# Kernel tuning notes

Hardware: AMD Instinct MI355X
Metric: run time of the kernel (lower is better)

## Reference

```python
import jax, jax.numpy as jnp
import numpy as np
import math

BT, N, D, H = 16, 1024, 128, 8
HD = D // H


def setup_inputs() -> dict:
    key = jax.random.key(0)
    ks = jax.random.split(key, 12)
    s = 1.0 / math.sqrt(D)
    return {
        "x": jax.random.normal(ks[0], (BT, N, D), dtype=jnp.float32),
        "adj": jax.random.uniform(ks[1], (BT, N, N), dtype=jnp.float32),
        "Wq": jax.random.normal(ks[2], (D, D), dtype=jnp.float32) * s,
        "bq": jax.random.normal(ks[3], (D,), dtype=jnp.float32) * 0.01,
        "Wk": jax.random.normal(ks[4], (D, D), dtype=jnp.float32) * s,
        "bk": jax.random.normal(ks[5], (D,), dtype=jnp.float32) * 0.01,
        "Wv": jax.random.normal(ks[6], (D, D), dtype=jnp.float32) * s,
        "bv": jax.random.normal(ks[7], (D,), dtype=jnp.float32) * 0.01,
        "Wo": jax.random.normal(ks[8], (D, D), dtype=jnp.float32) * s,
        "bo": jax.random.normal(ks[9], (D,), dtype=jnp.float32) * 0.01,
    }


def reference(x, adj, Wq, bq, Wk, bk, Wv, bv, Wo, bo):
    bt, n, d = x.shape
    # projections (torch Linear: x @ W.T + b), split into heads -> (BT,H,N,HD)
    q = (x @ Wq.T + bq).reshape(bt, n, H, HD).transpose(0, 2, 1, 3)
    k = (x @ Wk.T + bk).reshape(bt, n, H, HD).transpose(0, 2, 1, 3)
    v = (x @ Wv.T + bv).reshape(bt, n, H, HD).transpose(0, 2, 1, 3)
    scores = jnp.einsum('bhnd,bhmd->bhnm', q, k) / math.sqrt(HD)  # (BT,H,N,N)
    mask = (adj == 0)[:, None, :, :]  # (BT,1,N,N)
    scores = jnp.where(mask, -jnp.inf, scores)
    attn = jax.nn.softmax(scores, axis=-1)
    attn = attn * adj[:, None, :, :]  # reweight by continuous causal strength
    attn = attn / (attn.sum(axis=-1, keepdims=True) + 1e-8)  # renormalize
    ctx = jnp.einsum('bhnm,bhmd->bhnd', attn, v)  # (BT,H,N,HD)
    ctx = ctx.transpose(0, 2, 1, 3).reshape(bt, n, d)
    return ctx @ Wo.T + bo
```

## Files before the change

### kernel.cpp

```cpp
#include <hip/hip_runtime.h>
#include <hip/hip_bf16.h>

#define BTC 16
#define NC 1024
#define DC 128
#define HC 8
#define HDC 16

typedef __attribute__((ext_vector_type(8))) short bf16x8;
typedef __attribute__((ext_vector_type(4))) float f32x4;
typedef __attribute__((ext_vector_type(16))) float f32x16;
typedef __attribute__((ext_vector_type(4))) short short4v;

#if __has_builtin(__builtin_amdgcn_exp2f)
#define EXP2F(x) __builtin_amdgcn_exp2f(x)
#else
#define EXP2F(x) exp2f(x)
#endif

#define QSCALE 0.36067376022224085f

union PK2 { short4v s4; __hip_bfloat162 h2[2]; };
union PK8 { bf16x8 v; short s[8]; __hip_bfloat162 h2[4]; };

static __device__ inline short f2bf(float f) {
    unsigned u = __builtin_bit_cast(unsigned, f);
    u += 0x7fffu + ((u >> 16) & 1u);
    return (short)(u >> 16);
}

#define LDS_BARRIER()                                              \
    do {                                                           \
        asm volatile("s_waitcnt lgkmcnt(0)" ::: "memory");         \
        __builtin_amdgcn_s_barrier();                              \
        asm volatile("" ::: "memory");                             \
    } while (0)

__global__ __launch_bounds__(256)
void prep_kernel(const float* __restrict__ x,
                 const float* __restrict__ Wq, const float* __restrict__ Wk,
                 const float* __restrict__ Wv, const float* __restrict__ Wo,
                 short* __restrict__ xbf, short* __restrict__ Wbf)
{
    int gid  = blockIdx.x * 256 + threadIdx.x;
    int base = gid * 4;
    const float* src;
    short* dst;
    if (base < 2097152) {
        src = x + base; dst = xbf + base;
    } else {
        int idx = base - 2097152;
        int w   = idx >> 14;
        int off = idx & 16383;
        src = ((w == 0) ? Wq : (w == 1) ? Wk : (w == 2) ? Wv : Wo) + off;
        dst = Wbf + w * 16384 + off;
    }
    float4 v = *(const float4*)src;
    PK2 pk;
    pk.h2[0] = __float22bfloat162_rn(make_float2(v.x, v.y));
    pk.h2[1] = __float22bfloat162_rn(make_float2(v.z, v.w));
    *(short4v*)dst = pk.s4;
}

__global__ __launch_bounds__(256)
void proj_qkv(const short* __restrict__ xbf, const short* __restrict__ Wbf,
              const float* __restrict__ bq, const float* __restrict__ bk,
              const float* __restrict__ bv,
              short* __restrict__ qo, short* __restrict__ ko, short* __restrict__ vto)
{
    __shared__ short T[128 * 72];

    const int y = blockIdx.y;
    const short* W = Wbf + y * 16384;
    const float* bias = (y == 0) ? bq : (y == 1) ? bk : bv;
    const float scale = (y == 0) ? QSCALE : 1.0f;

    const int tid  = threadIdx.x;
    const int wave = tid >> 6;
    const int lane = tid & 63;
    const int l15  = lane & 15;
    const int quad = lane >> 4;
    const int rowA = blockIdx.x * 64 + wave * 16;

    f32x4 acc[8];
#pragma unroll
    for (int t = 0; t < 8; ++t) acc[t] = (f32x4){0.f, 0.f, 0.f, 0.f};

#pragma unroll
    for (int kk = 0; kk < DC; kk += 32) {
        bf16x8 Af = *(const bf16x8*)&xbf[(size_t)(rowA + l15) * DC + kk + quad * 8];
#pragma unroll
        for (int t = 0; t < 8; ++t) {
            bf16x8 Bf = *(const bf16x8*)&W[(t * 16 + l15) * DC + kk + quad * 8];
            acc[t] = __builtin_amdgcn_mfma_f32_16x16x32_bf16(Af, Bf, acc[t], 0, 0, 0);
        }
    }

    if (y == 2) {
#pragma unroll
        for (int t = 0; t < 8; ++t) {
            int c = t * 16 + l15;
            float b = bias[c];
            PK2 pk;
            pk.h2[0] = __float22bfloat162_rn(make_float2(acc[t][0] + b, acc[t][1] + b));
            pk.h2[1] = __float22bfloat162_rn(make_float2(acc[t][2] + b, acc[t][3] + b));
            *(short4v*)&T[c * 72 + wave * 16 + quad * 4] = pk.s4;
        }
        __syncthreads();
        const int bt = blockIdx.x >> 4;
        const int n0 = (blockIdx.x * 64) & 1023;
        const int chunk = tid & 7;
        const int dr    = tid >> 3;
#pragma unroll
        for (int rep = 0; rep < 4; ++rep) {
            int d = rep * 32 + dr;
            bf16x8 u = *(const bf16x8*)&T[d * 72 + chunk * 8];
            *(bf16x8*)&vto[((size_t)bt * DC + d) * NC + n0 + chunk * 8] = u;
        }
    } else {
        short* dst = (y == 0) ? qo : ko;
#pragma unroll
        for (int t = 0; t < 8; ++t) {
            int c  = t * 16 + l15;
            int hh = c >> 4, dd = c & 15;
            float b = bias[c];
#pragma unroll
            for (int r = 0; r < 4; ++r) {
                int row = rowA + quad * 4 + r;
                int btq = row >> 10, n = row & 1023;
                float val = (acc[t][r] + b) * scale;
                dst[(((size_t)btq * HC + hh) * NC + n) * HDC + dd] = f2bf(val);
            }
        }
    }
}

__global__ __launch_bounds__(256)
void proj_out(const short* __restrict__ cbf, const short* __restrict__ Wobf,
              const float* __restrict__ bo, float* __restrict__ out)
{
    const int tid  = threadIdx.x;
    const int wave = tid >> 6;
    const int lane = tid & 63;
    const int l15  = lane & 15;
    const int quad = lane >> 4;
    const int rowA = blockIdx.x * 64 + wave * 16;

    f32x4 acc[8];
#pragma unroll
    for (int t = 0; t < 8; ++t) acc[t] = (f32x4){0.f, 0.f, 0.f, 0.f};

#pragma unroll
    for (int kk = 0; kk < DC; kk += 32) {
        bf16x8 Af = *(const bf16x8*)&cbf[(size_t)(rowA + l15) * DC + kk + quad * 8];
#pragma unroll
        for (int t = 0; t < 8; ++t) {
            bf16x8 Bf = *(const bf16x8*)&Wobf[(t * 16 + l15) * DC + kk + quad * 8];
            acc[t] = __builtin_amdgcn_mfma_f32_16x16x32_bf16(Af, Bf, acc[t], 0, 0, 0);
        }
    }

#pragma unroll
    for (int t = 0; t < 8; ++t) {
        int c = t * 16 + l15;
        float b = bo[c];
#pragma unroll
        for (int r = 0; r < 4; ++r) {
            int row = rowA + quad * 4 + r;
            out[(size_t)row * DC + c] = acc[t][r] + b;
        }
    }
}

__global__ __launch_bounds__(256, 4)
void attn_kernel(const short* __restrict__ qh, const short* __restrict__ kh,
                 const short* __restrict__ vt, const float* __restrict__ adj,
                 short* __restrict__ cb)
{
    __shared__ float As[2][32 * 36];
    __shared__ short Ps[4][2][32 * 40];

    const int tid  = threadIdx.x;
    const int wave = tid >> 6;
    const int lane = tid & 63;
    const int l31  = lane & 31;
    const int hi   = lane >> 5;
    const int l15  = lane & 15;
    const int quad = lane >> 4;
    const int bt   = blockIdx.y;
    const int qt0  = blockIdx.x * 32;
    const int h    = blockIdx.z * 4 + wave;

    const size_t xb = (size_t)bt * NC * DC;
    const size_t hb = ((size_t)bt * HC + h) * NC;

    const short* kp = kh + (hb + l31) * HDC + hi * 8;
    const short* vp = vt + ((size_t)bt * DC + h * HDC + l15) * NC;
    const bf16x8 Bq = *(const bf16x8*)&qh[(hb + qt0 + l31) * HDC + hi * 8];

    const int arow = tid >> 3;
    const int acol = (tid & 7) * 4;
    const float* aptr = adj + (size_t)bt * NC * NC + (size_t)(qt0 + arow) * NC + acol;
    const int awoff = arow * 36 + acol;

    PK8 ones;
#pragma unroll
    for (int j = 0; j < 8; ++j) ones.s[j] = (short)0x3F80;

    f32x16 Z16;
#pragma unroll
    for (int i = 0; i < 16; ++i) Z16[i] = 0.f;

    f32x4 Cc[2], Cw[2];
#pragma unroll
    for (int s = 0; s < 2; ++s) {
        Cc[s] = (f32x4){0.f, 0.f, 0.f, 0.f};
        Cw[s] = (f32x4){0.f, 0.f, 0.f, 0.f};
    }

    short* Pa = &Ps[wave][0][0];
    short* Pb = &Ps[wave][1][0];

    float4 ar = *(const float4*)aptr;
    bf16x8 Ak = *(const bf16x8*)&kp[0];
    bf16x8 Bv = *(const bf16x8*)&vp[quad * 8];
    bf16x8 Bvp;

#define EXPTILE(ASB, PDST)                                                    \
    do {                                                                      \
        const float* asb = (ASB) + l31 * 36 + hi * 4;                         \
        float4 a0 = *(const float4*)&asb[0];                                  \
        float4 a1 = *(const float4*)&asb[8];                                  \
        float4 a2 = *(const float4*)&asb[16];                                 \
        float4 a3 = *(const float4*)&asb[24];                                 \
        short* pd = (PDST) + l31 * 40 + hi * 4;                               \
        PK2 pk;                                                               \
        pk.h2[0] = __float22bfloat162_rn(                                     \
            make_float2(EXP2F(S[0]) * a0.x, EXP2F(S[1]) * a0.y));             \
        pk.h2[1] = __float22bfloat162_rn(                                     \
            make_float2(EXP2F(S[2]) * a0.z, EXP2F(S[3]) * a0.w));             \
        *(short4v*)&pd[0] = pk.s4;                                            \
        pk.h2[0] = __float22bfloat162_rn(                                     \
            make_float2(EXP2F(S[4]) * a1.x, EXP2F(S[5]) * a1.y));             \
        pk.h2[1] = __float22bfloat162_rn(                                     \
            make_float2(EXP2F(S[6]) * a1.z, EXP2F(S[7]) * a1.w));             \
        *(short4v*)&pd[8] = pk.s4;                                            \
        pk.h2[0] = __float22bfloat162_rn(                                     \
            make_float2(EXP2F(S[8]) * a2.x, EXP2F(S[9]) * a2.y));             \
        pk.h2[1] = __float22bfloat162_rn(                                     \
            make_float2(EXP2F(S[10]) * a2.z, EXP2F(S[11]) * a2.w));           \
        *(short4v*)&pd[16] = pk.s4;                                           \
        pk.h2[0] = __float22bfloat162_rn(                                     \
            make_float2(EXP2F(S[12]) * a3.x, EXP2F(S[13]) * a3.y));           \
        pk.h2[1] = __float22bfloat162_rn(                                     \
            make_float2(EXP2F(S[14]) * a3.z, EXP2F(S[15]) * a3.w));           \
        *(short4v*)&pd[24] = pk.s4;                                           \
    } while (0)

    *(float4*)((char*)&As[0][0] + 0 + awoff * 4) = ar;
    ar = *(const float4*)(aptr + 32);
    LDS_BARRIER();

    {
        *(float4*)&As[1][awoff] = ar;
        ar = *(const float4*)(aptr + 64);
        bf16x8 Akn = *(const bf16x8*)&kp[32 * HDC];
        bf16x8 Bvn = *(const bf16x8*)&vp[32 + quad * 8];
        f32x16 S = __builtin_amdgcn_mfma_f32_32x32x16_bf16(Ak, Bq, Z16, 0, 0, 0);
        EXPTILE(&As[0][0], Pa);
        LDS_BARRIER();
        { short* t = Pa; Pa = Pb; Pb = t; }
        Ak = Akn; Bvp = Bv; Bv = Bvn;
    }

#pragma unroll 2
    for (int it = 1; it < 32; ++it) {
        const int jt  = it * 32;
        const int cur = it & 1;

        *(float4*)&As[cur ^ 1][awoff] = ar;
        ar = *(const float4*)(aptr + ((jt + 64) & (NC - 1)));

        bf16x8 Akn = *(const bf16x8*)&kp[((jt + 32) & (NC - 1)) * HDC];
        bf16x8 Bvn = *(const bf16x8*)&vp[((jt + 32) & (NC - 1)) + quad * 8];

        bf16x8 Ap0 = *(const bf16x8*)&Pb[l15 * 40 + quad * 8];
        bf16x8 Ap1 = *(const bf16x8*)&Pb[(16 + l15) * 40 + quad * 8];

        f32x16 S = __builtin_amdgcn_mfma_f32_32x32x16_bf16(Ak, Bq, Z16, 0, 0, 0);

        __builtin_amdgcn_s_setprio(1);
        Cc[0] = __builtin_amdgcn_mfma_f32_16x16x32_bf16(Ap0, Bvp, Cc[0], 0, 0, 0);
        Cw[0] = __builtin_amdgcn_mfma_f32_16x16x32_bf16(Ap0, ones.v, Cw[0], 0, 0, 0);
        Cc[1] = __builtin_amdgcn_mfma_f32_16x16x32_bf16(Ap1, Bvp, Cc[1], 0, 0, 0);
        Cw[1] = __builtin_amdgcn_mfma_f32_16x16x32_bf16(Ap1, ones.v, Cw[1], 0, 0, 0);
        __builtin_amdgcn_s_setprio(0);

        EXPTILE(&As[cur][0], Pa);
        LDS_BARRIER();

        { short* t = Pa; Pa = Pb; Pb = t; }
        Ak = Akn; Bvp = Bv; Bv = Bvn;
    }

    {
        bf16x8 Ap0 = *(const bf16x8*)&Pb[l15 * 40 + quad * 8];
        bf16x8 Ap1 = *(const bf16x8*)&Pb[(16 + l15) * 40 + quad * 8];
        Cc[0] = __builtin_amdgcn_mfma_f32_16x16x32_bf16(Ap0, Bvp, Cc[0], 0, 0, 0);
        Cw[0] = __builtin_amdgcn_mfma_f32_16x16x32_bf16(Ap0, ones.v, Cw[0], 0, 0, 0);
        Cc[1] = __builtin_amdgcn_mfma_f32_16x16x32_bf16(Ap1, Bvp, Cc[1], 0, 0, 0);
        Cw[1] = __builtin_amdgcn_mfma_f32_16x16x32_bf16(Ap1, ones.v, Cw[1], 0, 0, 0);
    }

#pragma unroll
    for (int s = 0; s < 2; ++s)
#pragma unroll
        for (int r = 0; r < 4; ++r) {
            float den = Cw[s][r];
            float rcp = den > 0.f ? 1.f / den : 0.f;
            int row = qt0 + s * 16 + quad * 4 + r;
            cb[xb + (size_t)row * DC + h * HDC + l15] = f2bf(Cc[s][r] * rcp);
        }
#undef EXPTILE
}

extern "C" void kernel_launch(void* const* d_in, const int* in_sizes, int n_in,
                              void* d_out, int out_size, void* d_ws, size_t ws_size,
                              hipStream_t stream)
{
    const float* x   = (const float*)d_in[0];
    const float* adj = (const float*)d_in[1];
    const float* Wq  = (const float*)d_in[2];
    const float* bq  = (const float*)d_in[3];
    const float* Wk  = (const float*)d_in[4];
    const float* bk  = (const float*)d_in[5];
    const float* Wv  = (const float*)d_in[6];
    const float* bv  = (const float*)d_in[7];
    const float* Wo  = (const float*)d_in[8];
    const float* bo  = (const float*)d_in[9];
    float* out = (float*)d_out;

    const size_t tok = (size_t)BTC * NC * DC;
    short* xbf  = (short*)d_ws;
    short* Wbf  = xbf  + tok;
    short* qbuf = Wbf  + 65536;
    short* kbuf = qbuf + tok;
    short* vt   = kbuf + tok;
    short* cbuf = vt   + tok;

    prep_kernel<<<2112, 256, 0, stream>>>(x, Wq, Wk, Wv, Wo, xbf, Wbf);

    dim3 pgrid(256, 3);
    proj_qkv<<<pgrid, 256, 0, stream>>>(xbf, Wbf, bq, bk, bv, qbuf, kbuf, vt);

    dim3 agrid(32, 16, 2);
    attn_kernel<<<agrid, 256, 0, stream>>>(qbuf, kbuf, vt, adj, cbuf);

    proj_out<<<256, 256, 0, stream>>>(cbuf, Wbf + 3 * 16384, bo, out);
}
```

Before: 174.6 us.

## Process 64-key tiles per iteration with single P buffer and fewer barriers

Widens the attention inner loop from 32 to 64 keys per iteration. It computes two score MFMAs and two exp tiles per step and halves the iteration count, and with it the number of LDS barriers. The double-buffered P tile becomes a single wider per-wave buffer. V fragments are now loaded within the same iteration instead of being prefetched one step ahead, and the adj prefetch distance changes. This raises register and LDS use per block, which may reduce occupancy or expose V load latency.

```diff
diff --git a/kernel.cpp b/kernel.cpp
--- a/kernel.cpp
+++ b/kernel.cpp
@@ -177,8 +177,8 @@
                  const short* __restrict__ vt, const float* __restrict__ adj,
                  short* __restrict__ cb)
 {
-    __shared__ float As[2][32 * 36];
-    __shared__ short Ps[4][2][32 * 40];
+    __shared__ float As[2][32 * 68];
+    __shared__ short Ps[4][32 * 72];
 
     const int tid  = threadIdx.x;
     const int wave = tid >> 6;
@@ -199,9 +199,9 @@
     const bf16x8 Bq = *(const bf16x8*)&qh[(hb + qt0 + l31) * HDC + hi * 8];
 
     const int arow = tid >> 3;
-    const int acol = (tid & 7) * 4;
-    const float* aptr = adj + (size_t)bt * NC * NC + (size_t)(qt0 + arow) * NC + acol;
-    const int awoff = arow * 36 + acol;
+    const int acolf = (tid & 7) * 8;
+    const float* aptr = adj + (size_t)bt * NC * NC + (size_t)(qt0 + arow) * NC + acolf;
+    const int awoff = arow * 68 + acolf;
 
     PK8 ones;
 #pragma unroll
@@ -218,22 +218,16 @@
         Cw[s] = (f32x4){0.f, 0.f, 0.f, 0.f};
     }
 
-    short* Pa = &Ps[wave][0][0];
-    short* Pb = &Ps[wave][1][0];
-
-    float4 ar = *(const float4*)aptr;
-    bf16x8 Ak = *(const bf16x8*)&kp[0];
-    bf16x8 Bv = *(const bf16x8*)&vp[quad * 8];
-    bf16x8 Bvp;
-
-#define EXPTILE(ASB, PDST)                                                    \
+    short* Pw = &Ps[wave][0];
+
+#define EXPTILE(S, ASB, H2)                                                   \
     do {                                                                      \
-        const float* asb = (ASB) + l31 * 36 + hi * 4;                         \
+        const float* asb = (ASB) + l31 * 68 + (H2) + hi * 4;                  \
         float4 a0 = *(const float4*)&asb[0];                                  \
         float4 a1 = *(const float4*)&asb[8];                                  \
         float4 a2 = *(const float4*)&asb[16];                                 \
         float4 a3 = *(const float4*)&asb[24];                                 \
-        short* pd = (PDST) + l31 * 40 + hi * 4;                               \
+        short* pd = Pw + l31 * 72 + (H2) + hi * 4;                            \
         PK2 pk;                                                               \
         pk.h2[0] = __float22bfloat162_rn(                                     \
             make_float2(EXP2F(S[0]) * a0.x, EXP2F(S[1]) * a0.y));             \
@@ -257,59 +251,90 @@
         *(short4v*)&pd[24] = pk.s4;                                           \
     } while (0)
 
-    *(float4*)((char*)&As[0][0] + 0 + awoff * 4) = ar;
-    ar = *(const float4*)(aptr + 32);
+    float4 p0a = *(const float4*)&aptr[0];
+    float4 p0b = *(const float4*)&aptr[4];
+    float4 ara = *(const float4*)&aptr[64];
+    float4 arb = *(const float4*)&aptr[68];
+    bf16x8 AkA = *(const bf16x8*)&kp[0];
+    bf16x8 AkB = *(const bf16x8*)&kp[32 * HDC];
+
+    *(float4*)((char*)&As[0][0] + awoff * 4)      = p0a;
+    *(float4*)((char*)&As[0][0] + awoff * 4 + 16) = p0b;
     LDS_BARRIER();
 
     {
-        *(float4*)&As[1][awoff] = ar;
-        ar = *(const float4*)(aptr + 64);
-        bf16x8 Akn = *(const bf16x8*)&kp[32 * HDC];
-        bf16x8 Bvn = *(const bf16x8*)&vp[32 + quad * 8];
-        f32x16 S = __builtin_amdgcn_mfma_f32_32x32x16_bf16(Ak, Bq, Z16, 0, 0, 0);
-        EXPTILE(&As[0][0], Pa);
+        float4 arna = *(const float4*)&aptr[128];
+        float4 arnb = *(const float4*)&aptr[132];
+        bf16x8 AkAn = *(const bf16x8*)&kp[64 * HDC];
+        bf16x8 AkBn = *(const bf16x8*)&kp[96 * HDC];
+
+        f32x16 S0 = __builtin_amdgcn_mfma_f32_32x32x16_bf16(AkA, Bq, Z16, 0, 0, 0);
+        EXPTILE(S0, &As[0][0], 0);
+        f32x16 S1 = __builtin_amdgcn_mfma_f32_32x32x16_bf16(AkB, Bq, Z16, 0, 0, 0);
+        EXPTILE(S1, &As[0][0], 32);
+
+        *(float4*)((char*)&As[1][0] + awoff * 4)      = ara;
+        *(float4*)((char*)&As[1][0] + awoff * 4 + 16) = arb;
         LDS_BARRIER();
-        { short* t = Pa; Pa = Pb; Pb = t; }
-        Ak = Akn; Bvp = Bv; Bv = Bvn;
-    }
-
-#pragma unroll 2
-    for (int it = 1; it < 32; ++it) {
-        const int jt  = it * 32;
+
+        ara = arna; arb = arnb; AkA = AkAn; AkB = AkBn;
+    }
+
+    for (int it = 1; it < 16; ++it) {
+        const int jt  = it * 64;
         const int cur = it & 1;
 
-        *(float4*)&As[cur ^ 1][awoff] = ar;
-        ar = *(const float4*)(aptr + ((jt + 64) & (NC - 1)));
-
-        bf16x8 Akn = *(const bf16x8*)&kp[((jt + 32) & (NC - 1)) * HDC];
-        bf16x8 Bvn = *(const bf16x8*)&vp[((jt + 32) & (NC - 1)) + quad * 8];
-
-        bf16x8 Ap0 = *(const bf16x8*)&Pb[l15 * 40 + quad * 8];
-        bf16x8 Ap1 = *(const bf16x8*)&Pb[(16 + l15) * 40 + quad * 8];
-
-        f32x16 S = __builtin_amdgcn_mfma_f32_32x32x16_bf16(Ak, Bq, Z16, 0, 0, 0);
+        bf16x8 ApA0 = *(const bf16x8*)&Pw[l15 * 72 + quad * 8];
+        bf16x8 ApA1 = *(const bf16x8*)&Pw[(16 + l15) * 72 + quad * 8];
+        bf16x8 ApB0 = *(const bf16x8*)&Pw[l15 * 72 + 32 + quad * 8];
+        bf16x8 ApB1 = *(const bf16x8*)&Pw[(16 + l15) * 72 + 32 + quad * 8];
+        bf16x8 BvpA = *(const bf16x8*)&vp[jt - 64 + quad * 8];
+        bf16x8 BvpB = *(const bf16x8*)&vp[jt - 32 + quad * 8];
+        const int nj2 = (jt + 128) & (NC - 1);
+        float4 arna = *(const float4*)&aptr[nj2];
+        float4 arnb = *(const float4*)&aptr[nj2 + 4];
+        bf16x8 AkAn = *(const bf16x8*)&kp[((jt + 64) & (NC - 1)) * HDC];
+        bf16x8 AkBn = *(const bf16x8*)&kp[((jt + 96) & (NC - 1)) * HDC];
+
+        f32x16 S0 = __builtin_amdgcn_mfma_f32_32x32x16_bf16(AkA, Bq, Z16, 0, 0, 0);
 
         __builtin_amdgcn_s_setprio(1);
-        Cc[0] = __builtin_amdgcn_mfma_f32_16x16x32_bf16(Ap0, Bvp, Cc[0], 0, 0, 0);
-        Cw[0] = __builtin_amdgcn_mfma_f32_16x16x32_bf16(Ap0, ones.v, Cw[0], 0, 0, 0);
-        Cc[1] = __builtin_amdgcn_mfma_f32_16x16x32_bf16(Ap1, Bvp, Cc[1], 0, 0, 0);
-        Cw[1] = __builtin_amdgcn_mfma_f32_16x16x32_bf16(Ap1, ones.v, Cw[1], 0, 0, 0);
+        Cc[0] = __builtin_amdgcn_mfma_f32_16x16x32_bf16(ApA0, BvpA, Cc[0], 0, 0, 0);
+        Cw[0] = __builtin_amdgcn_mfma_f32_16x16x32_bf16(ApA0, ones.v, Cw[0], 0, 0, 0);
+        Cc[1] = __builtin_amdgcn_mfma_f32_16x16x32_bf16(ApA1, BvpA, Cc[1], 0, 0, 0);
+        Cw[1] = __builtin_amdgcn_mfma_f32_16x16x32_bf16(ApA1, ones.v, Cw[1], 0, 0, 0);
+        Cc[0] = __builtin_amdgcn_mfma_f32_16x16x32_bf16(ApB0, BvpB, Cc[0], 0, 0, 0);
+        Cw[0] = __builtin_amdgcn_mfma_f32_16x16x32_bf16(ApB0, ones.v, Cw[0], 0, 0, 0);
+        Cc[1] = __builtin_amdgcn_mfma_f32_16x16x32_bf16(ApB1, BvpB, Cc[1], 0, 0, 0);
+        Cw[1] = __builtin_amdgcn_mfma_f32_16x16x32_bf16(ApB1, ones.v, Cw[1], 0, 0, 0);
         __builtin_amdgcn_s_setprio(0);
 
-        EXPTILE(&As[cur][0], Pa);
+        EXPTILE(S0, &As[cur][0], 0);
+        f32x16 S1 = __builtin_amdgcn_mfma_f32_32x32x16_bf16(AkB, Bq, Z16, 0, 0, 0);
+        EXPTILE(S1, &As[cur][0], 32);
+
+        *(float4*)((char*)&As[cur ^ 1][0] + awoff * 4)      = ara;
+        *(float4*)((char*)&As[cur ^ 1][0] + awoff * 4 + 16) = arb;
         LDS_BARRIER();
 
-        { short* t = Pa; Pa = Pb; Pb = t; }
-        Ak = Akn; Bvp = Bv; Bv = Bvn;
+        ara = arna; arb = arnb; AkA = AkAn; AkB = AkBn;
     }
 
     {
-        bf16x8 Ap0 = *(const bf16x8*)&Pb[l15 * 40 + quad * 8];
-        bf16x8 Ap1 = *(const bf16x8*)&Pb[(16 + l15) * 40 + quad * 8];
-        Cc[0] = __builtin_amdgcn_mfma_f32_16x16x32_bf16(Ap0, Bvp, Cc[0], 0, 0, 0);
-        Cw[0] = __builtin_amdgcn_mfma_f32_16x16x32_bf16(Ap0, ones.v, Cw[0], 0, 0, 0);
-        Cc[1] = __builtin_amdgcn_mfma_f32_16x16x32_bf16(Ap1, Bvp, Cc[1], 0, 0, 0);
-        Cw[1] = __builtin_amdgcn_mfma_f32_16x16x32_bf16(Ap1, ones.v, Cw[1], 0, 0, 0);
+        bf16x8 ApA0 = *(const bf16x8*)&Pw[l15 * 72 + quad * 8];
+        bf16x8 ApA1 = *(const bf16x8*)&Pw[(16 + l15) * 72 + quad * 8];
+        bf16x8 ApB0 = *(const bf16x8*)&Pw[l15 * 72 + 32 + quad * 8];
+        bf16x8 ApB1 = *(const bf16x8*)&Pw[(16 + l15) * 72 + 32 + quad * 8];
+        bf16x8 BvpA = *(const bf16x8*)&vp[960 + quad * 8];
+        bf16x8 BvpB = *(const bf16x8*)&vp[992 + quad * 8];
+        Cc[0] = __builtin_amdgcn_mfma_f32_16x16x32_bf16(ApA0, BvpA, Cc[0], 0, 0, 0);
+        Cw[0] = __builtin_amdgcn_mfma_f32_16x16x32_bf16(ApA0, ones.v, Cw[0], 0, 0, 0);
+        Cc[1] = __builtin_amdgcn_mfma_f32_16x16x32_bf16(ApA1, BvpA, Cc[1], 0, 0, 0);
+        Cw[1] = __builtin_amdgcn_mfma_f32_16x16x32_bf16(ApA1, ones.v, Cw[1], 0, 0, 0);
+        Cc[0] = __builtin_amdgcn_mfma_f32_16x16x32_bf16(ApB0, BvpB, Cc[0], 0, 0, 0);
+        Cw[0] = __builtin_amdgcn_mfma_f32_16x16x32_bf16(ApB0, ones.v, Cw[0], 0, 0, 0);
+        Cc[1] = __builtin_amdgcn_mfma_f32_16x16x32_bf16(ApB1, BvpB, Cc[1], 0, 0, 0);
+        Cw[1] = __builtin_amdgcn_mfma_f32_16x16x32_bf16(ApB1, ones.v, Cw[1], 0, 0, 0);
     }
 
 #pragma unroll
```

Result: faster. 169.6 us (-2.9%).
